# Kernel tuning notes

Hardware: AMD Instinct MI355X
Metric: run time of the kernel (lower is better)

The kernel has to match this reference:

```python
import jax, jax.numpy as jnp
import numpy as np

B = 4096
N0 = 784          # MNIST input
L0 = 263          # fc0: Gather chain 784 -> 256 (ELU after each)
L2 = 121          # fc2: Gather chain 256 -> 12 (ELU after each); final Gather 12 -> 10 has no ELU


def _win3(x):
    # x: (B, N) -> (B, N-2, 3) sliding windows of width 3
    return jnp.stack([x[:, :-2], x[:, 1:-1], x[:, 2:]], axis=-1)


def setup_inputs() -> dict:
    key = jax.random.key(0)
    kx, k0, k1, k2, k3, k4 = jax.random.split(key, 6)
    s = 0.75  # keeps activation variance roughly stable through ~380 ELU glia layers
    x = jax.random.normal(kx, (B, N0), jnp.float32)
    W0 = jax.random.normal(k0, (L0, 782, 3), jnp.float32) * s
    m0 = np.arange(782)[None, :] < (780 - 2 * np.arange(L0))[:, None]
    W0 = W0 * jnp.asarray(m0[..., None], jnp.float32)  # zero out rows past each layer's out size
    Ws = jax.random.normal(k1, (256, 3), jnp.float32) * s
    bs = jax.random.normal(k2, (256,), jnp.float32) * 0.1
    W2 = jax.random.normal(k3, (L2, 254, 3), jnp.float32) * s
    m2 = np.arange(254)[None, :] < (252 - 2 * np.arange(L2))[:, None]
    W2 = W2 * jnp.asarray(m2[..., None], jnp.float32)
    Wlast = jax.random.normal(k4, (10, 3), jnp.float32) * s
    return {"x": x, "W0": W0, "Ws": Ws, "bs": bs, "W2": W2, "Wlast": Wlast}


def reference(x, W0, Ws, bs, W2, Wlast):
    def gather_step(h, W):
        # locally-connected width-3 Gather (out = in - 2, bias=False) + ELU.
        # Invalid tail rows of W are zero, so padded positions stay exactly 0
        # (ELU(0)=0) and never contaminate valid windows.
        y = jax.nn.elu(jnp.einsum('bjk,jk->bj', _win3(h), W))
        return jnp.pad(y, ((0, 0), (0, 2))), None

    # fc0: 263 Gather+ELU layers, 784 -> 256 (valid prefix of fixed-width state)
    h, _ = jax.lax.scan(gather_step, x, W0)
    h = h[:, :256]
    # fc1: Slide(256) + ELU -- same-size width-3 locally connected layer, zero-padded window, bias
    hp = jnp.pad(h, ((0, 0), (1, 1)))
    h = jax.nn.elu(jnp.einsum('bjk,jk->bj', _win3(hp), Ws) + bs)
    # fc2: 121 Gather+ELU layers, 256 -> 12
    h, _ = jax.lax.scan(gather_step, h, W2)
    # final Gather(12): 12 -> 10, no ELU
    logits = jnp.einsum('bjk,jk->bj', _win3(h[:, :12]), Wlast)
    return jax.nn.log_softmax(logits, axis=1)
```

## Files before the change

kernel.cpp:

```cpp
#include <hip/hip_runtime.h>
#include <math.h>


#define G 2
#define BUFF4 576

template<int HI>
__device__ __forceinline__ float2 pk_mul_b(float2 a, float2 w) {
    float2 d;
    if constexpr (HI)
        asm("v_pk_mul_f32 %0, %1, %2 op_sel:[0,1] op_sel_hi:[1,1]"
            : "=v"(d) : "v"(a), "v"(w));
    else
        asm("v_pk_mul_f32 %0, %1, %2 op_sel_hi:[1,0]"
            : "=v"(d) : "v"(a), "v"(w));
    return d;
}
template<int HI>
__device__ __forceinline__ float2 pk_fma_b(float2 a, float2 w, float2 c) {
    float2 d;
    if constexpr (HI)
        asm("v_pk_fma_f32 %0, %1, %2, %3 op_sel:[0,1,0] op_sel_hi:[1,1,1]"
            : "=v"(d) : "v"(a), "v"(w), "v"(c));
    else
        asm("v_pk_fma_f32 %0, %1, %2, %3 op_sel_hi:[1,0,1]"
            : "=v"(d) : "v"(a), "v"(w), "v"(c));
    return d;
}
__device__ __forceinline__ float2 pk_mul2(float2 a, float2 b) {
    float2 d;
    asm("v_pk_mul_f32 %0, %1, %2" : "=v"(d) : "v"(a), "v"(b));
    return d;
}
__device__ __forceinline__ float vexp2(float x) {
    float d;
    asm("v_exp_f32 %0, %1" : "=v"(d) : "v"(x));
    return d;
}
__device__ __forceinline__ float med3z(float a, float em1) {
    float d;
    asm("v_med3_f32 %0, %1, %2, 0" : "=v"(d) : "v"(a), "v"(em1));
    return d;
}

__device__ __forceinline__ float elu_f(float a) {
    return a > 0.0f ? a : (__expf(a) - 1.0f);
}

__device__ __forceinline__ void gl2lds16(const float4* g, float4* l) {
    __builtin_amdgcn_global_load_lds(
        (const __attribute__((address_space(1))) unsigned int*)(const void*)g,
        (__attribute__((address_space(3))) unsigned int*)(void*)l, 16, 0, 0);
}

template<int K, int I, int NW>
__device__ __forceinline__ void slot_run(float2 (&h)[K], const float2 (&w)[NW],
                                         float2 e0, float2 e1, float2 l2e) {
    if constexpr (I < K) {
        float2 x1, x2;
        if constexpr (I + 1 < K) x1 = h[I + 1]; else x1 = e0;
        if constexpr (I + 2 < K) x2 = h[I + 2];
        else if constexpr (I + 2 == K) x2 = e0;
        else x2 = e1;
        float2 acc = pk_mul_b<(3 * I + 2) & 1>(x2, w[(3 * I + 2) >> 1]);
        acc = pk_fma_b<(3 * I + 1) & 1>(x1, w[(3 * I + 1) >> 1], acc);
        acc = pk_fma_b<(3 * I) & 1>(h[I], w[(3 * I) >> 1], acc);
        float2 t = pk_mul2(acc, l2e);
        float ex = vexp2(t.x) - 1.0f;
        float ey = vexp2(t.y) - 1.0f;
        h[I].x = med3z(acc.x, ex);
        h[I].y = med3z(acc.y, ey);
        slot_run<K, I + 1, NW>(h, w, e0, e1, l2e);
    }
}

template<int K, int NW>
__device__ __forceinline__ void scan_layer_pk(float2 (&h)[K], const float2 (&w)[NW],
                                              float2 l2e) {
    float2 e0, e1;
    e0.x = __shfl_down(h[0].x, 1); e0.y = __shfl_down(h[0].y, 1);
    if constexpr (K >= 2) { e1.x = __shfl_down(h[1].x, 1); e1.y = __shfl_down(h[1].y, 1); }
    else                  { e1.x = __shfl_down(h[0].x, 2); e1.y = __shfl_down(h[0].y, 2); }
    slot_run<K, 0, NW>(h, w, e0, e1, l2e);
}

template<int NC>
__device__ __forceinline__ void load_wt2(float2 (&w)[2 * NC], const float4* __restrict__ Tp,
                                         int lr) {
#pragma unroll
    for (int c = 0; c < NC; ++c) {
        float4 v = Tp[(size_t)lr * (NC * 64) + c * 64];
        w[2 * c]     = make_float2(v.x, v.y);
        w[2 * c + 1] = make_float2(v.z, v.w);
    }
}

template<int K, int NC, int NL>
__device__ __forceinline__ void scan_direct(const float* __restrict__ Tph, int lane,
                                            float2 (&h)[K], float2 l2e) {
    const float4* __restrict__ Tp = reinterpret_cast<const float4*>(Tph) + lane;
    for (int l = 0; l < NL; ++l) {
        float2 w[2 * NC];
        load_wt2<NC>(w, Tp, l);
        scan_layer_pk<K>(h, w, l2e);
    }
}

template<int NC>
__device__ __forceinline__ void prefetch_layer0(const float* __restrict__ Tph, int lane,
                                                float4* dst) {
    const float4* src = reinterpret_cast<const float4*>(Tph) + lane;
#pragma unroll
    for (int c = 0; c < NC; ++c) gl2lds16(src + c * 64, dst + c * 64);
}

template<int K, int NC, int NL, int NNC>
__device__ __forceinline__ void scan_phase_lds(const float* __restrict__ Tph,
                                               const float* __restrict__ Tnext,
                                               int lane, float2 (&h)[K], float2 l2e,
                                               float4* pool, int& cur) {
    const float4* __restrict__ Tp = reinterpret_cast<const float4*>(Tph) + lane;
    for (int l = 0; l < NL; ++l) {
        float4* dst = pool + (cur ^ 1) * BUFF4;
        if (l + 1 < NL) {
            const float4* src = Tp + (size_t)(l + 1) * (NC * 64);
#pragma unroll
            for (int c = 0; c < NC; ++c) gl2lds16(src + c * 64, dst + c * 64);
        } else if constexpr (NNC > 0) {
            const float4* src = reinterpret_cast<const float4*>(Tnext) + lane;
#pragma unroll
            for (int c = 0; c < NNC; ++c) gl2lds16(src + c * 64, dst + c * 64);
        }
        const float4* wsrc = pool + cur * BUFF4 + lane;
        float2 w[2 * NC];
#pragma unroll
        for (int c = 0; c < NC; ++c) {
            float4 v = wsrc[(size_t)c * 64];
            w[2 * c]     = make_float2(v.x, v.y);
            w[2 * c + 1] = make_float2(v.z, v.w);
        }
        scan_layer_pk<K>(h, w, l2e);
        asm volatile("s_waitcnt vmcnt(0)" ::: "memory");
        __builtin_amdgcn_sched_barrier(0);
        cur ^= 1;
    }
}

template<int KA, int KB>
__device__ __forceinline__ void repack_w(float2 (&a)[KA], float2 (&n)[KB],
                                         float2* scratch, int lane) {
#pragma unroll
    for (int i = 0; i < KA; ++i) scratch[KA * lane + i] = a[i];
    asm volatile("s_waitcnt lgkmcnt(0)" ::: "memory");
    __builtin_amdgcn_sched_barrier(0);
#pragma unroll
    for (int i = 0; i < KB; ++i) n[i] = scratch[KB * lane + i];
    asm volatile("s_waitcnt lgkmcnt(0)" ::: "memory");
    __builtin_amdgcn_sched_barrier(0);
}

__device__ __forceinline__ void stage2_pk(float2 (&h)[5], const float* __restrict__ Ws,
                                          const float* __restrict__ bs, int lane) {
#pragma unroll
    for (int i = 0; i < 5; ++i)
        if (5 * lane + i > 255) h[i] = make_float2(0.f, 0.f);
    float w0[5], w1[5], w2[5], bb[5];
#pragma unroll
    for (int i = 0; i < 5; ++i) {
        int j = 5 * lane + i;
        bool v = j < 256;
        w0[i] = v ? Ws[3 * j + 0] : 0.f;
        w1[i] = v ? Ws[3 * j + 1] : 0.f;
        w2[i] = v ? Ws[3 * j + 2] : 0.f;
        bb[i] = v ? bs[j] : 0.f;
    }
    float2 p, q;
    p.x = __shfl_up(h[4].x, 1); p.y = __shfl_up(h[4].y, 1);
    if (lane == 0) p = make_float2(0.f, 0.f);
    q.x = __shfl_down(h[0].x, 1); q.y = __shfl_down(h[0].y, 1);
    float2 y[5];
#pragma unroll
    for (int i = 0; i < 5; ++i) {
        float2 xm = (i == 0) ? p : h[i - 1];
        float2 xp = (i == 4) ? q : h[i + 1];
        float ax = fmaf(xm.x, w0[i], fmaf(h[i].x, w1[i], fmaf(xp.x, w2[i], bb[i])));
        float ay = fmaf(xm.y, w0[i], fmaf(h[i].y, w1[i], fmaf(xp.y, w2[i], bb[i])));
        y[i].x = elu_f(ax);
        y[i].y = elu_f(ay);
    }
#pragma unroll
    for (int i = 0; i < 5; ++i) h[i] = y[i];
}

__device__ __forceinline__ void emit_row(float v, const float* __restrict__ Wl,
                                         float* __restrict__ out, int row, int lane) {
    float n1 = __shfl_down(v, 1);
    float n2 = __shfl_down(v, 2);
    float lg = 0.0f;
    if (lane < 10)
        lg = fmaf(v, Wl[3 * lane], fmaf(n1, Wl[3 * lane + 1], n2 * Wl[3 * lane + 2]));
    float t = (lane < 10) ? lg : -1e30f;
#pragma unroll
    for (int d = 1; d < 16; d <<= 1) t = fmaxf(t, __shfl_xor(t, d));
    float e = (lane < 10) ? __expf(lg - t) : 0.0f;
    float s = e;
#pragma unroll
    for (int d = 1; d < 16; d <<= 1) s += __shfl_xor(s, d);
    float lse = t + __logf(s);
    if (lane < 10) out[(size_t)row * 10 + lane] = lg - lse;
}

#define T_TOTAL 531712
#define T_ALLOC (T_TOTAL + 512)

__global__ __launch_bounds__(256)
void reorder_w(const float* __restrict__ W0, const float* __restrict__ W2,
               float* __restrict__ T) {
    int idx = blockIdx.x * 256 + threadIdx.x;
    if (idx >= T_ALLOC) return;
    if (idx >= T_TOTAL) { T[idx] = 0.0f; return; }
    int base, l0, K, NC, s1;
    if      (idx < 17920)  { base = 0;      l0 = 0;   K = 13; NC = 10; s1 = 1; }
    else if (idx < 91648)  { base = 17920;  l0 = 7;   K = 12; NC = 9;  s1 = 1; }
    else if (idx < 165376) { base = 91648;  l0 = 39;  K = 11; NC = 9;  s1 = 1; }
    else if (idx < 230912) { base = 165376; l0 = 71;  K = 10; NC = 8;  s1 = 1; }
    else if (idx < 288256) { base = 230912; l0 = 103; K = 9;  NC = 7;  s1 = 1; }
    else if (idx < 337408) { base = 288256; l0 = 135; K = 8;  NC = 6;  s1 = 1; }
    else if (idx < 386560) { base = 337408; l0 = 167; K = 7;  NC = 6;  s1 = 1; }
    else if (idx < 427520) { base = 386560; l0 = 199; K = 6;  NC = 5;  s1 = 1; }
    else if (idx < 460288) { base = 427520; l0 = 231; K = 5;  NC = 4;  s1 = 1; }
    else if (idx < 484096) { base = 460288; l0 = 0;   K = 4;  NC = 3;  s1 = 0; }
    else if (idx < 508672) { base = 484096; l0 = 31;  K = 3;  NC = 3;  s1 = 0; }
    else if (idx < 525056) { base = 508672; l0 = 63;  K = 2;  NC = 2;  s1 = 0; }
    else                   { base = 525056; l0 = 95;  K = 1;  NC = 1;  s1 = 0; }
    const float* Wsrc = s1 ? W0 : W2;
    int lstride = s1 ? 2346 : 762;
    int rel  = idx - base;
    int perL = NC * 256;
    int lr   = rel / perL;
    int r2   = rel - lr * perL;
    int c    = r2 >> 8;
    int ln   = (r2 >> 2) & 63;
    int f    = r2 & 3;
    int elem = 4 * c + f;
    float v = 0.0f;
    if (elem < 3 * K) {
        int b = 3 * K * ln;
        if (b + 3 * K > lstride) b = lstride - 3 * K;
        v = Wsrc[(size_t)(l0 + lr) * lstride + b + elem];
    }
    T[idx] = v;
}

__global__ __launch_bounds__(64)
void pg_kernel_pk(const float* __restrict__ x,  const float* __restrict__ Ws,
                  const float* __restrict__ bs, const float* __restrict__ Wlast,
                  const float* __restrict__ T,  float* __restrict__ out)
{
    __shared__ float4 pool[2 * BUFF4];
    const int lane = threadIdx.x;
    const int rowA = blockIdx.x * G;
    const int rowB = rowA + 1;
    const float2 l2e = make_float2(1.44269504088896340736f, 1.44269504088896340736f);

    float2 h13[13];
#pragma unroll
    for (int i = 0; i < 13; ++i) {
        int p = 13 * lane + i;
        h13[i].x = (p < 784) ? x[(size_t)rowA * 784 + p] : 0.0f;
        h13[i].y = (p < 784) ? x[(size_t)rowB * 784 + p] : 0.0f;
    }

    scan_direct<13, 10, 7>(T + 0, lane, h13, l2e);
    int cur = 0;
    prefetch_layer0<9>(T + 17920, lane, pool + 0);
    float2 h12[12];
    repack_w<13, 12>(h13, h12, (float2*)(pool + BUFF4), lane);
    asm volatile("s_waitcnt vmcnt(0)" ::: "memory");
    __builtin_amdgcn_sched_barrier(0);

    scan_phase_lds<12, 9, 32, 9>(T + 17920,  T + 91648,  lane, h12, l2e, pool, cur);
    float2 h11[11]; repack_w<12, 11>(h12, h11, (float2*)(pool + (cur ^ 1) * BUFF4), lane);
    scan_phase_lds<11, 9, 32, 8>(T + 91648,  T + 165376, lane, h11, l2e, pool, cur);
    float2 h10[10]; repack_w<11, 10>(h11, h10, (float2*)(pool + (cur ^ 1) * BUFF4), lane);
    scan_phase_lds<10, 8, 32, 7>(T + 165376, T + 230912, lane, h10, l2e, pool, cur);
    float2 h9[9];   repack_w<10, 9>(h10, h9, (float2*)(pool + (cur ^ 1) * BUFF4), lane);
    scan_phase_lds<9, 7, 32, 6>(T + 230912,  T + 288256, lane, h9, l2e, pool, cur);
    float2 h8[8];   repack_w<9, 8>(h9, h8, (float2*)(pool + (cur ^ 1) * BUFF4), lane);
    scan_phase_lds<8, 6, 32, 6>(T + 288256,  T + 337408, lane, h8, l2e, pool, cur);
    float2 h7[7];   repack_w<8, 7>(h8, h7, (float2*)(pool + (cur ^ 1) * BUFF4), lane);
    scan_phase_lds<7, 6, 32, 5>(T + 337408,  T + 386560, lane, h7, l2e, pool, cur);
    float2 h6[6];   repack_w<7, 6>(h7, h6, (float2*)(pool + (cur ^ 1) * BUFF4), lane);
    scan_phase_lds<6, 5, 32, 4>(T + 386560,  T + 427520, lane, h6, l2e, pool, cur);
    float2 h5[5];   repack_w<6, 5>(h6, h5, (float2*)(pool + (cur ^ 1) * BUFF4), lane);
    scan_phase_lds<5, 4, 32, 3>(T + 427520,  T + 460288, lane, h5, l2e, pool, cur);

    stage2_pk(h5, Ws, bs, lane);

    float2 h4[4];   repack_w<5, 4>(h5, h4, (float2*)(pool + (cur ^ 1) * BUFF4), lane);
    scan_phase_lds<4, 3, 31, 3>(T + 460288,  T + 484096, lane, h4, l2e, pool, cur);
    float2 h3[3];   repack_w<4, 3>(h4, h3, (float2*)(pool + (cur ^ 1) * BUFF4), lane);
    scan_phase_lds<3, 3, 32, 2>(T + 484096,  T + 508672, lane, h3, l2e, pool, cur);
    float2 h2[2];   repack_w<3, 2>(h3, h2, (float2*)(pool + (cur ^ 1) * BUFF4), lane);
    scan_phase_lds<2, 2, 32, 1>(T + 508672,  T + 525056, lane, h2, l2e, pool, cur);
    float2 h1[1];   repack_w<2, 1>(h2, h1, (float2*)(pool + (cur ^ 1) * BUFF4), lane);
    scan_phase_lds<1, 1, 26, 0>(T + 525056,  (const float*)0, lane, h1, l2e, pool, cur);

    emit_row(h1[0].x, Wlast, out, rowA, lane);
    emit_row(h1[0].y, Wlast, out, rowB, lane);
}

template<int K>
__device__ __forceinline__ void scan_layer_s(float (&h)[K], const float (&w)[3 * K]) {
    float e0 = __shfl_down(h[0], 1);
    float e1;
    if constexpr (K >= 2) e1 = __shfl_down(h[1], 1);
    else                  e1 = __shfl_down(h[0], 2);
#pragma unroll
    for (int i = 0; i < K; ++i) {
        float x1 = (i + 1 < K) ? h[i + 1] : e0;
        float x2 = (i + 2 < K) ? h[i + 2] : ((i + 2 == K) ? e0 : e1);
        float a = fmaf(h[i], w[3 * i], fmaf(x1, w[3 * i + 1], x2 * w[3 * i + 2]));
        h[i] = elu_f(a);
    }
}
template<int K>
__device__ __forceinline__ void scan_phase_s(const float* __restrict__ W, int lstride,
                                             int l0, int l1, int lane,
                                             float (&hA)[K], float (&hB)[K]) {
    int base = 3 * K * lane;
    if (base + 3 * K > lstride) base = lstride - 3 * K;
    const float* __restrict__ Wp = W + (size_t)l0 * lstride + base;
    float wa[3 * K];
    for (int l = l0; l < l1; ++l) {
#pragma unroll
        for (int j = 0; j < 3 * K; ++j) wa[j] = Wp[j];
        scan_layer_s<K>(hA, wa);
        scan_layer_s<K>(hB, wa);
        Wp += lstride;
    }
}
template<int KA, int KB>
__device__ __forceinline__ void repack_s(float (&aA)[KA], float (&aB)[KA],
                                         float (&nA)[KB], float (&nB)[KB],
                                         float* lds, int lane) {
    __syncthreads();
#pragma unroll
    for (int i = 0; i < KA; ++i) lds[KA * lane + i] = aA[i];
    __syncthreads();
#pragma unroll
    for (int i = 0; i < KB; ++i) nA[i] = lds[KB * lane + i];
    __syncthreads();
#pragma unroll
    for (int i = 0; i < KA; ++i) lds[KA * lane + i] = aB[i];
    __syncthreads();
#pragma unroll
    for (int i = 0; i < KB; ++i) nB[i] = lds[KB * lane + i];
    __syncthreads();
}
__global__ __launch_bounds__(64)
void pg_kernel_d(const float* __restrict__ x,  const float* __restrict__ W0,
                 const float* __restrict__ Ws, const float* __restrict__ bs,
                 const float* __restrict__ W2, const float* __restrict__ Wlast,
                 float* __restrict__ out)
{
    __shared__ float lds[13 * 64];
    const int lane = threadIdx.x;
    const int rowA = blockIdx.x * 2;
    const int rowB = rowA + 1;
    float a13[13], b13[13];
#pragma unroll
    for (int i = 0; i < 13; ++i) {
        int p = 13 * lane + i;
        a13[i] = (p < 784) ? x[(size_t)rowA * 784 + p] : 0.0f;
        b13[i] = (p < 784) ? x[(size_t)rowB * 784 + p] : 0.0f;
    }
    scan_phase_s<13>(W0, 2346, 0, 71, lane, a13, b13);
    float a10[10], b10[10]; repack_s<13, 10>(a13, b13, a10, b10, lds, lane);
    scan_phase_s<10>(W0, 2346, 71, 167, lane, a10, b10);
    float a7[7], b7[7];     repack_s<10, 7>(a10, b10, a7, b7, lds, lane);
    scan_phase_s<7>(W0, 2346, 167, 231, lane, a7, b7);
    float a5[5], b5[5];     repack_s<7, 5>(a7, b7, a5, b5, lds, lane);
    scan_phase_s<5>(W0, 2346, 231, 263, lane, a5, b5);
    {
        float2 hp[5];
#pragma unroll
        for (int i = 0; i < 5; ++i) hp[i] = make_float2(a5[i], b5[i]);
        stage2_pk(hp, Ws, bs, lane);
#pragma unroll
        for (int i = 0; i < 5; ++i) { a5[i] = hp[i].x; b5[i] = hp[i].y; }
    }
    float a4[4], b4[4];     repack_s<5, 4>(a5, b5, a4, b4, lds, lane);
    scan_phase_s<4>(W2, 762, 0, 31, lane, a4, b4);
    float a3[3], b3[3];     repack_s<4, 3>(a4, b4, a3, b3, lds, lane);
    scan_phase_s<3>(W2, 762, 31, 63, lane, a3, b3);
    float a2_[2], b2_[2];   repack_s<3, 2>(a3, b3, a2_, b2_, lds, lane);
    scan_phase_s<2>(W2, 762, 63, 95, lane, a2_, b2_);
    float a1[1], b1[1];     repack_s<2, 1>(a2_, b2_, a1, b1, lds, lane);
    scan_phase_s<1>(W2, 762, 95, 121, lane, a1, b1);
    emit_row(a1[0], Wlast, out, rowA, lane);
    emit_row(b1[0], Wlast, out, rowB, lane);
}

extern "C" void kernel_launch(void* const* d_in, const int* in_sizes, int n_in,
                              void* d_out, int out_size, void* d_ws, size_t ws_size,
                              hipStream_t stream) {
    const float* x     = (const float*)d_in[0];
    const float* W0    = (const float*)d_in[1];
    const float* Ws    = (const float*)d_in[2];
    const float* bs    = (const float*)d_in[3];
    const float* W2    = (const float*)d_in[4];
    const float* Wlast = (const float*)d_in[5];
    float* out = (float*)d_out;

    if (ws_size >= (size_t)T_ALLOC * sizeof(float)) {
        float* T = (float*)d_ws;
        reorder_w<<<(T_ALLOC + 255) / 256, 256, 0, stream>>>(W0, W2, T);
        pg_kernel_pk<<<4096 / G, 64, 0, stream>>>(x, Ws, bs, Wlast, T, out);
    } else {
        pg_kernel_d<<<2048, 64, 0, stream>>>(x, W0, Ws, bs, W2, Wlast, out);
    }
}
```

Before: 277.8 us.

## Share weight staging across four waves per block with cooperative LDS prefetch

Result: slower. 296.5 us (+6.7%).

```diff
diff --git a/kernel.cpp b/kernel.cpp
--- a/kernel.cpp
+++ b/kernel.cpp
@@ -2,8 +2,7 @@
 #include <math.h>
 
 
-#define G 2
-#define BUFF4 576
+#define BUFF4 640
 
 template<int HI>
 __device__ __forceinline__ float2 pk_mul_b(float2 a, float2 w) {
@@ -42,7 +41,6 @@
     asm("v_med3_f32 %0, %1, %2, 0" : "=v"(d) : "v"(a), "v"(em1));
     return d;
 }
-
 __device__ __forceinline__ float elu_f(float a) {
     return a > 0.0f ? a : (__expf(a) - 1.0f);
 }
@@ -84,64 +82,36 @@
     slot_run<K, 0, NW>(h, w, e0, e1, l2e);
 }
 
-template<int NC>
-__device__ __forceinline__ void load_wt2(float2 (&w)[2 * NC], const float4* __restrict__ Tp,
-                                         int lr) {
-#pragma unroll
-    for (int c = 0; c < NC; ++c) {
-        float4 v = Tp[(size_t)lr * (NC * 64) + c * 64];
-        w[2 * c]     = make_float2(v.x, v.y);
-        w[2 * c + 1] = make_float2(v.z, v.w);
-    }
-}
-
-template<int K, int NC, int NL>
-__device__ __forceinline__ void scan_direct(const float* __restrict__ Tph, int lane,
-                                            float2 (&h)[K], float2 l2e) {
-    const float4* __restrict__ Tp = reinterpret_cast<const float4*>(Tph) + lane;
-    for (int l = 0; l < NL; ++l) {
-        float2 w[2 * NC];
-        load_wt2<NC>(w, Tp, l);
-        scan_layer_pk<K>(h, w, l2e);
-    }
-}
-
-template<int NC>
-__device__ __forceinline__ void prefetch_layer0(const float* __restrict__ Tph, int lane,
-                                                float4* dst) {
-    const float4* src = reinterpret_cast<const float4*>(Tph) + lane;
-#pragma unroll
-    for (int c = 0; c < NC; ++c) gl2lds16(src + c * 64, dst + c * 64);
-}
-
 template<int K, int NC, int NL, int NNC>
-__device__ __forceinline__ void scan_phase_lds(const float* __restrict__ Tph,
-                                               const float* __restrict__ Tnext,
-                                               int lane, float2 (&h)[K], float2 l2e,
-                                               float4* pool, int& cur) {
-    const float4* __restrict__ Tp = reinterpret_cast<const float4*>(Tph) + lane;
+__device__ __forceinline__ void scan_phase4(const float* __restrict__ Tph,
+                                            const float* __restrict__ Tnext,
+                                            int w, int lane,
+                                            float2 (&h)[K], float2 l2e,
+                                            float4* pool, int& cur) {
     for (int l = 0; l < NL; ++l) {
         float4* dst = pool + (cur ^ 1) * BUFF4;
         if (l + 1 < NL) {
-            const float4* src = Tp + (size_t)(l + 1) * (NC * 64);
-#pragma unroll
-            for (int c = 0; c < NC; ++c) gl2lds16(src + c * 64, dst + c * 64);
+            const float4* src = reinterpret_cast<const float4*>(Tph)
+                              + (size_t)(l + 1) * (NC * 64);
+#pragma unroll
+            for (int c = 0; c < NC; ++c)
+                if ((c & 3) == w) gl2lds16(src + c * 64 + lane, dst + c * 64 + lane);
         } else if constexpr (NNC > 0) {
-            const float4* src = reinterpret_cast<const float4*>(Tnext) + lane;
-#pragma unroll
-            for (int c = 0; c < NNC; ++c) gl2lds16(src + c * 64, dst + c * 64);
+            const float4* src = reinterpret_cast<const float4*>(Tnext);
+#pragma unroll
+            for (int c = 0; c < NNC; ++c)
+                if ((c & 3) == w) gl2lds16(src + c * 64 + lane, dst + c * 64 + lane);
         }
-        const float4* wsrc = pool + cur * BUFF4 + lane;
-        float2 w[2 * NC];
+        const float4* wsrc = pool + cur * BUFF4;
+        float2 wr[2 * NC];
 #pragma unroll
         for (int c = 0; c < NC; ++c) {
-            float4 v = wsrc[(size_t)c * 64];
-            w[2 * c]     = make_float2(v.x, v.y);
-            w[2 * c + 1] = make_float2(v.z, v.w);
+            float4 v = wsrc[c * 64 + lane];
+            wr[2 * c]     = make_float2(v.x, v.y);
+            wr[2 * c + 1] = make_float2(v.z, v.w);
         }
-        scan_layer_pk<K>(h, w, l2e);
-        asm volatile("s_waitcnt vmcnt(0)" ::: "memory");
-        __builtin_amdgcn_sched_barrier(0);
+        scan_layer_pk<K>(h, wr, l2e);
+        __syncthreads();
         cur ^= 1;
     }
 }
@@ -211,14 +181,12 @@
 }
 
 #define T_TOTAL 531712
-#define T_ALLOC (T_TOTAL + 512)
 
 __global__ __launch_bounds__(256)
 void reorder_w(const float* __restrict__ W0, const float* __restrict__ W2,
                float* __restrict__ T) {
     int idx = blockIdx.x * 256 + threadIdx.x;
-    if (idx >= T_ALLOC) return;
-    if (idx >= T_TOTAL) { T[idx] = 0.0f; return; }
+    if (idx >= T_TOTAL) return;
     int base, l0, K, NC, s1;
     if      (idx < 17920)  { base = 0;      l0 = 0;   K = 13; NC = 10; s1 = 1; }
     else if (idx < 91648)  { base = 17920;  l0 = 7;   K = 12; NC = 9;  s1 = 1; }
@@ -252,16 +220,27 @@
     T[idx] = v;
 }
 
-__global__ __launch_bounds__(64)
-void pg_kernel_pk(const float* __restrict__ x,  const float* __restrict__ Ws,
+__global__ __launch_bounds__(256)
+void pg_kernel_4w(const float* __restrict__ x,  const float* __restrict__ Ws,
                   const float* __restrict__ bs, const float* __restrict__ Wlast,
                   const float* __restrict__ T,  float* __restrict__ out)
 {
     __shared__ float4 pool[2 * BUFF4];
-    const int lane = threadIdx.x;
-    const int rowA = blockIdx.x * G;
+    __shared__ float2 scr[4 * 13 * 64];
+    const int tid  = threadIdx.x;
+    const int w    = tid >> 6;
+    const int lane = tid & 63;
+    const int rowA = blockIdx.x * 8 + 2 * w;
     const int rowB = rowA + 1;
+    float2* scratch = scr + w * (13 * 64);
     const float2 l2e = make_float2(1.44269504088896340736f, 1.44269504088896340736f);
+
+    {
+        const float4* src = reinterpret_cast<const float4*>(T);
+#pragma unroll
+        for (int c = 0; c < 10; ++c)
+            if ((c & 3) == w) gl2lds16(src + c * 64 + lane, pool + c * 64 + lane);
+    }
 
     float2 h13[13];
 #pragma unroll
@@ -270,41 +249,37 @@
         h13[i].x = (p < 784) ? x[(size_t)rowA * 784 + p] : 0.0f;
         h13[i].y = (p < 784) ? x[(size_t)rowB * 784 + p] : 0.0f;
     }
-
-    scan_direct<13, 10, 7>(T + 0, lane, h13, l2e);
+    __syncthreads();
     int cur = 0;
-    prefetch_layer0<9>(T + 17920, lane, pool + 0);
-    float2 h12[12];
-    repack_w<13, 12>(h13, h12, (float2*)(pool + BUFF4), lane);
-    asm volatile("s_waitcnt vmcnt(0)" ::: "memory");
-    __builtin_amdgcn_sched_barrier(0);
-
-    scan_phase_lds<12, 9, 32, 9>(T + 17920,  T + 91648,  lane, h12, l2e, pool, cur);
-    float2 h11[11]; repack_w<12, 11>(h12, h11, (float2*)(pool + (cur ^ 1) * BUFF4), lane);
-    scan_phase_lds<11, 9, 32, 8>(T + 91648,  T + 165376, lane, h11, l2e, pool, cur);
-    float2 h10[10]; repack_w<11, 10>(h11, h10, (float2*)(pool + (cur ^ 1) * BUFF4), lane);
-    scan_phase_lds<10, 8, 32, 7>(T + 165376, T + 230912, lane, h10, l2e, pool, cur);
-    float2 h9[9];   repack_w<10, 9>(h10, h9, (float2*)(pool + (cur ^ 1) * BUFF4), lane);
-    scan_phase_lds<9, 7, 32, 6>(T + 230912,  T + 288256, lane, h9, l2e, pool, cur);
-    float2 h8[8];   repack_w<9, 8>(h9, h8, (float2*)(pool + (cur ^ 1) * BUFF4), lane);
-    scan_phase_lds<8, 6, 32, 6>(T + 288256,  T + 337408, lane, h8, l2e, pool, cur);
-    float2 h7[7];   repack_w<8, 7>(h8, h7, (float2*)(pool + (cur ^ 1) * BUFF4), lane);
-    scan_phase_lds<7, 6, 32, 5>(T + 337408,  T + 386560, lane, h7, l2e, pool, cur);
-    float2 h6[6];   repack_w<7, 6>(h7, h6, (float2*)(pool + (cur ^ 1) * BUFF4), lane);
-    scan_phase_lds<6, 5, 32, 4>(T + 386560,  T + 427520, lane, h6, l2e, pool, cur);
-    float2 h5[5];   repack_w<6, 5>(h6, h5, (float2*)(pool + (cur ^ 1) * BUFF4), lane);
-    scan_phase_lds<5, 4, 32, 3>(T + 427520,  T + 460288, lane, h5, l2e, pool, cur);
+
+    scan_phase4<13, 10, 7, 9>(T + 0,       T + 17920,  w, lane, h13, l2e, pool, cur);
+    float2 h12[12]; repack_w<13, 12>(h13, h12, scratch, lane);
+    scan_phase4<12, 9, 32, 9>(T + 17920,   T + 91648,  w, lane, h12, l2e, pool, cur);
+    float2 h11[11]; repack_w<12, 11>(h12, h11, scratch, lane);
+    scan_phase4<11, 9, 32, 8>(T + 91648,   T + 165376, w, lane, h11, l2e, pool, cur);
+    float2 h10[10]; repack_w<11, 10>(h11, h10, scratch, lane);
+    scan_phase4<10, 8, 32, 7>(T + 165376,  T + 230912, w, lane, h10, l2e, pool, cur);
+    float2 h9[9];   repack_w<10, 9>(h10, h9, scratch, lane);
+    scan_phase4<9, 7, 32, 6>(T + 230912,   T + 288256, w, lane, h9, l2e, pool, cur);
+    float2 h8[8];   repack_w<9, 8>(h9, h8, scratch, lane);
+    scan_phase4<8, 6, 32, 6>(T + 288256,   T + 337408, w, lane, h8, l2e, pool, cur);
+    float2 h7[7];   repack_w<8, 7>(h8, h7, scratch, lane);
+    scan_phase4<7, 6, 32, 5>(T + 337408,   T + 386560, w, lane, h7, l2e, pool, cur);
+    float2 h6[6];   repack_w<7, 6>(h7, h6, scratch, lane);
+    scan_phase4<6, 5, 32, 4>(T + 386560,   T + 427520, w, lane, h6, l2e, pool, cur);
+    float2 h5[5];   repack_w<6, 5>(h6, h5, scratch, lane);
+    scan_phase4<5, 4, 32, 3>(T + 427520,   T + 460288, w, lane, h5, l2e, pool, cur);
 
     stage2_pk(h5, Ws, bs, lane);
 
-    float2 h4[4];   repack_w<5, 4>(h5, h4, (float2*)(pool + (cur ^ 1) * BUFF4), lane);
-    scan_phase_lds<4, 3, 31, 3>(T + 460288,  T + 484096, lane, h4, l2e, pool, cur);
-    float2 h3[3];   repack_w<4, 3>(h4, h3, (float2*)(pool + (cur ^ 1) * BUFF4), lane);
-    scan_phase_lds<3, 3, 32, 2>(T + 484096,  T + 508672, lane, h3, l2e, pool, cur);
-    float2 h2[2];   repack_w<3, 2>(h3, h2, (float2*)(pool + (cur ^ 1) * BUFF4), lane);
-    scan_phase_lds<2, 2, 32, 1>(T + 508672,  T + 525056, lane, h2, l2e, pool, cur);
-    float2 h1[1];   repack_w<2, 1>(h2, h1, (float2*)(pool + (cur ^ 1) * BUFF4), lane);
-    scan_phase_lds<1, 1, 26, 0>(T + 525056,  (const float*)0, lane, h1, l2e, pool, cur);
+    float2 h4[4];   repack_w<5, 4>(h5, h4, scratch, lane);
+    scan_phase4<4, 3, 31, 3>(T + 460288,   T + 484096, w, lane, h4, l2e, pool, cur);
+    float2 h3[3];   repack_w<4, 3>(h4, h3, scratch, lane);
+    scan_phase4<3, 3, 32, 2>(T + 484096,   T + 508672, w, lane, h3, l2e, pool, cur);
+    float2 h2[2];   repack_w<3, 2>(h3, h2, scratch, lane);
+    scan_phase4<2, 2, 32, 1>(T + 508672,   T + 525056, w, lane, h2, l2e, pool, cur);
+    float2 h1[1];   repack_w<2, 1>(h2, h1, scratch, lane);
+    scan_phase4<1, 1, 26, 0>(T + 525056,   (const float*)0, w, lane, h1, l2e, pool, cur);
 
     emit_row(h1[0].x, Wlast, out, rowA, lane);
     emit_row(h1[0].y, Wlast, out, rowB, lane);
@@ -413,10 +388,10 @@
     const float* Wlast = (const float*)d_in[5];
     float* out = (float*)d_out;
 
-    if (ws_size >= (size_t)T_ALLOC * sizeof(float)) {
+    if (ws_size >= (size_t)T_TOTAL * sizeof(float)) {
         float* T = (float*)d_ws;
-        reorder_w<<<(T_ALLOC + 255) / 256, 256, 0, stream>>>(W0, W2, T);
-        pg_kernel_pk<<<4096 / G, 64, 0, stream>>>(x, Ws, bs, Wlast, T, out);
+        reorder_w<<<(T_TOTAL + 255) / 256, 256, 0, stream>>>(W0, W2, T);
+        pg_kernel_4w<<<512, 256, 0, stream>>>(x, Ws, bs, Wlast, T, out);
     } else {
         pg_kernel_d<<<2048, 64, 0, stream>>>(x, W0, Ws, bs, W2, Wlast, out);
     }
```
